# Kernel tuning notes

Measured on AMD Instinct MI355X. Metric: run time of the kernel, lower is better.

## Reference

```python
import jax, jax.numpy as jnp
import numpy as np


def setup_inputs() -> dict:
    key = jax.random.key(0)
    k1, k2, k3 = jax.random.split(key, 3)
    B, F, K = 16384, 512, 1000
    D = jax.random.normal(k1, (B, F), dtype=jnp.float32)
    weight = jax.random.normal(k2, (K, F), dtype=jnp.float32)  # (out_features, in_features)
    gamma = jax.random.uniform(k3, (K,), dtype=jnp.float32)
    return {"D": D, "weight": weight, "gamma": gamma}


def reference(D, weight, gamma):
    # Squared Euclidean distance from each row of D to each centroid (row of weight),
    # computed via ||a||^2 + ||b||^2 - 2 a.b (mathematically equal to the broadcast
    # subtract-square-sum in the original torch forward with d_view=None).
    d_sq = jnp.sum(D * D, axis=1, keepdims=True)            # (B, 1)
    w_sq = jnp.sum(weight * weight, axis=1)                  # (K,)
    cross = jnp.einsum('bf,kf->bk', D, weight)               # (B, K)
    dist_sq = d_sq + w_sq[None, :] - 2.0 * cross             # (B, K)
    return -dist_sq * gamma                                  # (B, K)
```

## Files before the change

### kernel.cpp

```cpp
#include <hip/hip_runtime.h>
#include <hip/hip_bf16.h>
#include <stdint.h>

#define B_ROWS 16384
#define F_DIM  512
#define K_OUT  1000
#define K_PAD  1024

#define BM 128
#define BN 128
#define BK 64

typedef __attribute__((ext_vector_type(4))) float f32x4;
typedef __attribute__((ext_vector_type(8))) short short8;
typedef unsigned short u16;
typedef unsigned int   u32;

#define OFF_WB   0
#define OFF_WSQ  1048576

__device__ __forceinline__ u16 f2bf(float f) {
  union { float f; u32 u; } v; v.f = f;
  u32 u = v.u;
  u32 r = (u + 0x7fffu + ((u >> 16) & 1u)) >> 16;
  return (u16)r;
}

__device__ __forceinline__ u32 pkbf(float lo, float hi) {
  u32 d;
  asm("v_cvt_pk_bf16_f32 %0, %1, %2" : "=v"(d) : "v"(lo), "v"(hi));
  return d;
}

__global__ void prep_W(const float* __restrict__ W, u16* __restrict__ Wb,
                       float* __restrict__ wsq) {
  int w    = threadIdx.x >> 6;
  int lane = threadIdx.x & 63;
  int row  = blockIdx.x * 4 + w;
  uint4 p; p.x = p.y = p.z = p.w = 0u;
  float s = 0.f;
  if (row < K_OUT) {
    const float* src = W + (size_t)row * F_DIM + lane * 8;
    float4 v0 = *(const float4*)src;
    float4 v1 = *(const float4*)(src + 4);
    s = v0.x*v0.x + v0.y*v0.y + v0.z*v0.z + v0.w*v0.w
      + v1.x*v1.x + v1.y*v1.y + v1.z*v1.z + v1.w*v1.w;
    p.x = (u32)f2bf(v0.x) | ((u32)f2bf(v0.y) << 16);
    p.y = (u32)f2bf(v0.z) | ((u32)f2bf(v0.w) << 16);
    p.z = (u32)f2bf(v1.x) | ((u32)f2bf(v1.y) << 16);
    p.w = (u32)f2bf(v1.z) | ((u32)f2bf(v1.w) << 16);
  }
#pragma unroll
  for (int off = 32; off >= 1; off >>= 1) s += __shfl_xor(s, off);
  if (lane == 0) wsq[row] = s;
  *(uint4*)(Wb + (size_t)row * F_DIM + lane * 8) = p;
}

__device__ __forceinline__ void gload_lds16(const void* g, void* l) {
  __builtin_amdgcn_global_load_lds(
      (const __attribute__((address_space(1))) void*)g,
      (__attribute__((address_space(3))) void*)l,
      16, 0, 0);
}


#define LOAD_A(kb)                                                             \
  _Pragma("unroll") for (int i = 0; i < 8; ++i) {                              \
    int r = w * 32 + i * 4 + r4;                                               \
    la[i] = *(const float4*)(Dg + (size_t)r * F_DIM + (kb) + gq * 4);          \
  }

#define WRITE_A(dstA)                                                          \
  _Pragma("unroll") for (int i = 0; i < 8; ++i) {                              \
    int r = w * 32 + i * 4 + r4;                                               \
    pa[i] += la[i].x*la[i].x + la[i].y*la[i].y                                 \
           + la[i].z*la[i].z + la[i].w*la[i].w;                                \
    uint2 q2; q2.x = pkbf(la[i].x, la[i].y); q2.y = pkbf(la[i].z, la[i].w);    \
    *(uint2*)((dstA) + r * 128 + (((gq >> 1) ^ (r & 7)) << 4) + (gq & 1) * 8)  \
        = q2;                                                                  \
  }

#define STAGE_B(q)                                                             \
  _Pragma("unroll") for (int j = 0; j < 2; ++j) {                              \
    int rb = (q) * 32 + j * 64 + w * 8;                                        \
    int r  = rb + (lane >> 3);                                                 \
    int sc = s8 ^ (r & 7);                                                     \
    gload_lds16(Bg + (size_t)r * F_DIM + kbn + sc * 8, sBn + rb * 128);        \
  }

__global__ __launch_bounds__(256, 2) void gemm_eps(
    const float* __restrict__ D,
    const u16*   __restrict__ Bw,
    const float* __restrict__ wsq,
    const float* __restrict__ gamma,
    float* __restrict__ out) {
  __shared__ __align__(16) char lds[66048];
  float* dsq_s = (float*)(lds + 65536);

  const int tid  = threadIdx.x;
  const int w    = tid >> 6;
  const int lane = tid & 63;
  const int lr   = lane & 15;
  const int lk4  = lane >> 4;
  const int wm   = w >> 1;
  const int wn   = w & 1;
  const int gq   = lane & 15;
  const int r4   = lane >> 4;
  const int s8   = lane & 7;

  const int bid = blockIdx.x;
  const int wg  = (bid & 7) * 128 + (bid >> 3);
  const int mt  = wg >> 3;
  const int nt  = wg & 7;
  const int m0  = mt * BM;
  const int n0  = nt * BN;

  const float* Dg = D  + (size_t)m0 * F_DIM;
  const u16*   Bg = Bw + (size_t)n0 * F_DIM;

  f32x4 acc[4][4];
#pragma unroll
  for (int i = 0; i < 4; ++i)
#pragma unroll
    for (int j = 0; j < 4; ++j) acc[i][j] = (f32x4){0.f, 0.f, 0.f, 0.f};
  float  pa[8] = {0.f, 0.f, 0.f, 0.f, 0.f, 0.f, 0.f, 0.f};
  float4 la[8];

  float g_[4], wq_[4];
#pragma unroll
  for (int ni = 0; ni < 4; ++ni) {
    int col = n0 + wn * 64 + ni * 16 + lr;
    g_[ni]  = (col < K_OUT) ? gamma[col] : 0.f;
    wq_[ni] = wsq[col & (K_PAD - 1)];
  }

  {
    char* sBn = lds + 32768;
    const int kbn = 0;
    LOAD_A(0)
    STAGE_B(0) STAGE_B(1)
    WRITE_A(lds)
    asm volatile("s_waitcnt lgkmcnt(0)" ::: "memory");
    __builtin_amdgcn_sched_barrier(0);
  }

#pragma unroll 2
  for (int t = 0; t < 8; ++t) {
    const char* sAc = lds + (t & 1) * 16384;
    const char* sBc = lds + 32768 + (t & 1) * 16384;
    char* sAn = lds + ((t + 1) & 1) * 16384;
    char* sBn = lds + 32768 + ((t + 1) & 1) * 16384;
    const int kbn = ((t + 1) & 7) * BK;

    LOAD_A(kbn)
    STAGE_B(0) STAGE_B(1)
    __builtin_amdgcn_sched_barrier(0);

    asm volatile("s_waitcnt vmcnt(12)" ::: "memory");
    __builtin_amdgcn_s_barrier();

    short8 a[2][4], b[2][4];
#pragma unroll
    for (int kk = 0; kk < 2; ++kk)
#pragma unroll
      for (int mi = 0; mi < 4; ++mi) {
        int rA = wm * 64 + mi * 16 + lr;
        a[kk][mi] = *(const short8*)(sAc + rA * 128 +
                                     ((((kk << 2) + lk4) ^ (rA & 7)) << 4));
        int rB = wn * 64 + mi * 16 + lr;
        b[kk][mi] = *(const short8*)(sBc + rB * 128 +
                                     ((((kk << 2) + lk4) ^ (rB & 7)) << 4));
      }

    __builtin_amdgcn_s_setprio(1);
#pragma unroll
    for (int kk = 0; kk < 2; ++kk)
#pragma unroll
      for (int mi = 0; mi < 4; ++mi)
#pragma unroll
        for (int ni = 0; ni < 4; ++ni)
          acc[mi][ni] = __builtin_amdgcn_mfma_f32_16x16x32_bf16(
              a[kk][mi], b[kk][ni], acc[mi][ni], 0, 0, 0);
    __builtin_amdgcn_s_setprio(0);
    __builtin_amdgcn_sched_barrier(0);

    if (t < 7) { WRITE_A(sAn) }
    asm volatile("s_waitcnt lgkmcnt(0)" ::: "memory");
    __builtin_amdgcn_sched_barrier(0);
    __builtin_amdgcn_s_barrier();
  }

#pragma unroll
  for (int i = 0; i < 8; ++i) {
    float s = pa[i];
    s += __shfl_xor(s, 1); s += __shfl_xor(s, 2);
    s += __shfl_xor(s, 4); s += __shfl_xor(s, 8);
    if (gq == 0) dsq_s[w * 32 + i * 4 + r4] = s;
  }
  __syncthreads();

  float4 dl[4];
#pragma unroll
  for (int mi = 0; mi < 4; ++mi)
    dl[mi] = *(const float4*)&dsq_s[wm * 64 + mi * 16 + lk4 * 4];

  float* ch = (float*)lds;
  const int rl = tid >> 3;
  const int cb = (tid & 7) << 2;
#pragma unroll
  for (int c = 0; c < 2; ++c) {
    __syncthreads();
    if (wm == c) {
#pragma unroll
      for (int mi = 0; mi < 4; ++mi) {
        const int row_l = mi * 16 + lk4 * 4;
#pragma unroll
        for (int j = 0; j < 4; ++j) {
          float dq = (j == 0) ? dl[mi].x : (j == 1) ? dl[mi].y
                   : (j == 2) ? dl[mi].z : dl[mi].w;
#pragma unroll
          for (int ni = 0; ni < 4; ++ni) {
            ch[(row_l + j) * 132 + wn * 64 + ni * 16 + lr] =
                g_[ni] * (2.f * acc[mi][ni][j] - dq - wq_[ni]);
          }
        }
      }
    }
    __syncthreads();
#pragma unroll
    for (int half = 0; half < 2; ++half) {
#pragma unroll
      for (int s = 0; s < 4; ++s) {
        int row = half * 32 + rl;
        int col = cb + s * 32;
        if (n0 + col < K_OUT) {
          float4 v = *(const float4*)&ch[row * 132 + col];
          *(float4*)&out[(size_t)(m0 + c * 64 + row) * K_OUT + n0 + col] = v;
        }
      }
    }
  }
}

extern "C" void kernel_launch(void* const* d_in, const int* in_sizes, int n_in,
                              void* d_out, int out_size, void* d_ws, size_t ws_size,
                              hipStream_t stream) {
  const float* D     = (const float*)d_in[0];
  const float* W     = (const float*)d_in[1];
  const float* gamma = (const float*)d_in[2];
  float* out = (float*)d_out;
  char*  ws  = (char*)d_ws;

  u16*   Wb  = (u16*)(ws + OFF_WB);
  float* wsq = (float*)(ws + OFF_WSQ);

  prep_W<<<K_PAD / 4, 256, 0, stream>>>(W, Wb, wsq);

  gemm_eps<<<(B_ROWS / BM) * (K_PAD / BN), 256, 0, stream>>>(
      D, Wb, wsq, gamma, out);
}
```

Baseline: 46.42 us.

## Stage fp32 A tiles directly to LDS via async loads, convert to bf16 at fragment read

```diff
diff --git a/kernel.cpp b/kernel.cpp
--- a/kernel.cpp
+++ b/kernel.cpp
@@ -9,7 +9,7 @@
 
 #define BM 128
 #define BN 128
-#define BK 64
+#define BK 32
 
 typedef __attribute__((ext_vector_type(4))) float f32x4;
 typedef __attribute__((ext_vector_type(8))) short short8;
@@ -18,6 +18,13 @@
 
 #define OFF_WB   0
 #define OFF_WSQ  1048576
+
+#define A0_OFF   0
+#define A1_OFF   16384
+#define B0_OFF   32768
+#define B1_OFF   40960
+#define DSQ_OFF  49152
+#define LDS_SZ   49664
 
 __device__ __forceinline__ u16 f2bf(float f) {
   union { float f; u32 u; } v; v.f = f;
@@ -64,38 +71,30 @@
 }
 
 
-#define LOAD_A(kb)                                                             \
-  _Pragma("unroll") for (int i = 0; i < 8; ++i) {                              \
-    int r = w * 32 + i * 4 + r4;                                               \
-    la[i] = *(const float4*)(Dg + (size_t)r * F_DIM + (kb) + gq * 4);          \
-  }
-
-#define WRITE_A(dstA)                                                          \
-  _Pragma("unroll") for (int i = 0; i < 8; ++i) {                              \
-    int r = w * 32 + i * 4 + r4;                                               \
-    pa[i] += la[i].x*la[i].x + la[i].y*la[i].y                                 \
-           + la[i].z*la[i].z + la[i].w*la[i].w;                                \
-    uint2 q2; q2.x = pkbf(la[i].x, la[i].y); q2.y = pkbf(la[i].z, la[i].w);    \
-    *(uint2*)((dstA) + r * 128 + (((gq >> 1) ^ (r & 7)) << 4) + (gq & 1) * 8)  \
-        = q2;                                                                  \
-  }
-
-#define STAGE_B(q)                                                             \
-  _Pragma("unroll") for (int j = 0; j < 2; ++j) {                              \
-    int rb = (q) * 32 + j * 64 + w * 8;                                        \
-    int r  = rb + (lane >> 3);                                                 \
+#define STAGE_A(g)                                                             \
+  {                                                                            \
+    int r  = (g) * 32 + w * 8 + ra8;                                           \
     int sc = s8 ^ (r & 7);                                                     \
-    gload_lds16(Bg + (size_t)r * F_DIM + kbn + sc * 8, sBn + rb * 128);        \
-  }
-
-__global__ __launch_bounds__(256, 2) void gemm_eps(
+    gload_lds16(Dg + (size_t)r * F_DIM + kbn + sc * 4,                         \
+                sAn + (g) * 4096 + w * 1024);                                  \
+  }
+
+#define STAGE_B(j)                                                             \
+  {                                                                            \
+    int r  = (j) * 64 + w * 16 + rb4;                                          \
+    int sc = s4 ^ (r & 3);                                                     \
+    gload_lds16(Bg + (size_t)r * F_DIM + kbn + sc * 8,                         \
+                sBn + (j) * 4096 + w * 1024);                                  \
+  }
+
+__global__ __launch_bounds__(256, 3) void gemm_eps(
     const float* __restrict__ D,
     const u16*   __restrict__ Bw,
     const float* __restrict__ wsq,
     const float* __restrict__ gamma,
     float* __restrict__ out) {
-  __shared__ __align__(16) char lds[66048];
-  float* dsq_s = (float*)(lds + 65536);
+  __shared__ __align__(16) char lds[LDS_SZ];
+  float* dsq_s = (float*)(lds + DSQ_OFF);
 
   const int tid  = threadIdx.x;
   const int w    = tid >> 6;
@@ -104,9 +103,10 @@
   const int lk4  = lane >> 4;
   const int wm   = w >> 1;
   const int wn   = w & 1;
-  const int gq   = lane & 15;
-  const int r4   = lane >> 4;
+  const int ra8  = lane >> 3;
   const int s8   = lane & 7;
+  const int rb4  = lane >> 2;
+  const int s4   = lane & 3;
 
   const int bid = blockIdx.x;
   const int wg  = (bid & 7) * 128 + (bid >> 3);
@@ -123,82 +123,80 @@
   for (int i = 0; i < 4; ++i)
 #pragma unroll
     for (int j = 0; j < 4; ++j) acc[i][j] = (f32x4){0.f, 0.f, 0.f, 0.f};
-  float  pa[8] = {0.f, 0.f, 0.f, 0.f, 0.f, 0.f, 0.f, 0.f};
-  float4 la[8];
+  float pa[4] = {0.f, 0.f, 0.f, 0.f};
+
+  {
+    char* sAn = lds + A0_OFF;
+    char* sBn = lds + B0_OFF;
+    const int kbn = 0;
+    STAGE_A(0) STAGE_A(1) STAGE_A(2) STAGE_A(3)
+    STAGE_B(0) STAGE_B(1)
+  }
+
+#pragma unroll 2
+  for (int t = 0; t < 16; ++t) {
+    const char* sAc = lds + ((t & 1) ? A1_OFF : A0_OFF);
+    const char* sBc = lds + ((t & 1) ? B1_OFF : B0_OFF);
+    char* sAn = lds + ((t & 1) ? A0_OFF : A1_OFF);
+    char* sBn = lds + ((t & 1) ? B0_OFF : B1_OFF);
+    const int kbn = ((t + 1) & 15) * BK;
+
+    STAGE_A(0) STAGE_A(1) STAGE_A(2) STAGE_A(3)
+    STAGE_B(0) STAGE_B(1)
+
+    asm volatile("s_waitcnt vmcnt(6)" ::: "memory");
+    __builtin_amdgcn_s_barrier();
+    asm volatile("" ::: "memory");
+
+    short8 a[4], b[4];
+#pragma unroll
+    for (int mi = 0; mi < 4; ++mi) {
+      int rA = wm * 64 + mi * 16 + lr;
+      const char* baseA = sAc + rA * 128;
+      float4 f0 = *(const float4*)(baseA + ((((lk4 << 1) | 0) ^ (rA & 7)) << 4));
+      float4 f1 = *(const float4*)(baseA + ((((lk4 << 1) | 1) ^ (rA & 7)) << 4));
+      union { uint4 u; short8 s; } cv;
+      cv.u.x = pkbf(f0.x, f0.y); cv.u.y = pkbf(f0.z, f0.w);
+      cv.u.z = pkbf(f1.x, f1.y); cv.u.w = pkbf(f1.z, f1.w);
+      a[mi] = cv.s;
+      if (wn == 0)
+        pa[mi] += f0.x*f0.x + f0.y*f0.y + f0.z*f0.z + f0.w*f0.w
+                + f1.x*f1.x + f1.y*f1.y + f1.z*f1.z + f1.w*f1.w;
+      int rB = wn * 64 + mi * 16 + lr;
+      b[mi] = *(const short8*)(sBc + rB * 64 + ((lk4 ^ (rB & 3)) << 4));
+    }
+
+    __builtin_amdgcn_s_setprio(1);
+#pragma unroll
+    for (int mi = 0; mi < 4; ++mi)
+#pragma unroll
+      for (int ni = 0; ni < 4; ++ni)
+        acc[mi][ni] = __builtin_amdgcn_mfma_f32_16x16x32_bf16(
+            a[mi], b[ni], acc[mi][ni], 0, 0, 0);
+    __builtin_amdgcn_s_setprio(0);
+
+    asm volatile("" ::: "memory");
+    __builtin_amdgcn_s_barrier();
+  }
+
+  if (wn == 0) {
+#pragma unroll
+    for (int mi = 0; mi < 4; ++mi) {
+      float s = pa[mi];
+      s += __shfl_xor(s, 16);
+      s += __shfl_xor(s, 32);
+      if (lk4 == 0) dsq_s[wm * 64 + mi * 16 + lr] = s;
+    }
+  }
+  __syncthreads();
 
   float g_[4], wq_[4];
 #pragma unroll
   for (int ni = 0; ni < 4; ++ni) {
     int col = n0 + wn * 64 + ni * 16 + lr;
     g_[ni]  = (col < K_OUT) ? gamma[col] : 0.f;
-    wq_[ni] = wsq[col & (K_PAD - 1)];
-  }
-
-  {
-    char* sBn = lds + 32768;
-    const int kbn = 0;
-    LOAD_A(0)
-    STAGE_B(0) STAGE_B(1)
-    WRITE_A(lds)
-    asm volatile("s_waitcnt lgkmcnt(0)" ::: "memory");
-    __builtin_amdgcn_sched_barrier(0);
-  }
-
-#pragma unroll 2
-  for (int t = 0; t < 8; ++t) {
-    const char* sAc = lds + (t & 1) * 16384;
-    const char* sBc = lds + 32768 + (t & 1) * 16384;
-    char* sAn = lds + ((t + 1) & 1) * 16384;
-    char* sBn = lds + 32768 + ((t + 1) & 1) * 16384;
-    const int kbn = ((t + 1) & 7) * BK;
-
-    LOAD_A(kbn)
-    STAGE_B(0) STAGE_B(1)
-    __builtin_amdgcn_sched_barrier(0);
-
-    asm volatile("s_waitcnt vmcnt(12)" ::: "memory");
-    __builtin_amdgcn_s_barrier();
-
-    short8 a[2][4], b[2][4];
-#pragma unroll
-    for (int kk = 0; kk < 2; ++kk)
-#pragma unroll
-      for (int mi = 0; mi < 4; ++mi) {
-        int rA = wm * 64 + mi * 16 + lr;
-        a[kk][mi] = *(const short8*)(sAc + rA * 128 +
-                                     ((((kk << 2) + lk4) ^ (rA & 7)) << 4));
-        int rB = wn * 64 + mi * 16 + lr;
-        b[kk][mi] = *(const short8*)(sBc + rB * 128 +
-                                     ((((kk << 2) + lk4) ^ (rB & 7)) << 4));
-      }
-
-    __builtin_amdgcn_s_setprio(1);
-#pragma unroll
-    for (int kk = 0; kk < 2; ++kk)
-#pragma unroll
-      for (int mi = 0; mi < 4; ++mi)
-#pragma unroll
-        for (int ni = 0; ni < 4; ++ni)
-          acc[mi][ni] = __builtin_amdgcn_mfma_f32_16x16x32_bf16(
-              a[kk][mi], b[kk][ni], acc[mi][ni], 0, 0, 0);
-    __builtin_amdgcn_s_setprio(0);
-    __builtin_amdgcn_sched_barrier(0);
-
-    if (t < 7) { WRITE_A(sAn) }
-    asm volatile("s_waitcnt lgkmcnt(0)" ::: "memory");
-    __builtin_amdgcn_sched_barrier(0);
-    __builtin_amdgcn_s_barrier();
-  }
-
-#pragma unroll
-  for (int i = 0; i < 8; ++i) {
-    float s = pa[i];
-    s += __shfl_xor(s, 1); s += __shfl_xor(s, 2);
-    s += __shfl_xor(s, 4); s += __shfl_xor(s, 8);
-    if (gq == 0) dsq_s[w * 32 + i * 4 + r4] = s;
-  }
-  __syncthreads();
-
+    wq_[ni] = wsq[col];
+  }
   float4 dl[4];
 #pragma unroll
   for (int mi = 0; mi < 4; ++mi)
```

Measured after the change: 52.87 us. +13.9%, slower.
